# Kernel optimization log

Measured on AMD Instinct MI355X. Metric: run time of the kernel, lower is better.

## Reference

```python
import jax, jax.numpy as jnp
import numpy as np

B, N, D, H = 4, 2048, 1024, 16
HD = D // H  # head_dim = 64


def setup_inputs() -> dict:
    key = jax.random.key(0)
    ks = jax.random.split(key, 7)
    q = jax.random.normal(ks[0], (B, N, D), dtype=jnp.float32)
    k = jax.random.normal(ks[1], (B, N, D), dtype=jnp.float32)
    v = jax.random.normal(ks[2], (B, N, D), dtype=jnp.float32)
    scale = 0.02
    Wq = jax.random.normal(ks[3], (D, D), dtype=jnp.float32) * scale
    Wk = jax.random.normal(ks[4], (D, D), dtype=jnp.float32) * scale
    Wv = jax.random.normal(ks[5], (D, D), dtype=jnp.float32) * scale
    Wo = jax.random.normal(ks[6], (D, D), dtype=jnp.float32) * scale
    return {"q": q, "k": k, "v": v, "Wq": Wq, "Wk": Wk, "Wv": Wv, "Wo": Wo}


def _split_heads(x):
    # b n (h d) -> b h n d
    b, n, d = x.shape
    return x.reshape(b, n, H, HD).transpose(0, 2, 1, 3)


def reference(q, k, v, Wq, Wk, Wv, Wo):
    # nn.Linear(bias=False): y = x @ W.T
    qh = _split_heads(q @ Wq.T)
    kh = _split_heads(k @ Wk.T)
    vh = _split_heads(v @ Wv.T)
    scale = jnp.sqrt(jnp.asarray(HD, dtype=jnp.float32))
    scores = jnp.einsum('bhqd,bhkd->bhqk', qh, kh) / scale  # [B,H,N,N]
    # future (causal) mask: triu(ones, diagonal=1) -> masked_fill(-inf)
    future_mask = jnp.triu(jnp.ones((N, N), dtype=bool), k=1)
    scores = jnp.where(future_mask[None, None, :, :], -jnp.inf, scores)
    attn = jax.nn.softmax(scores, axis=-1)
    out = jnp.einsum('bhqk,bhkd->bhqd', attn, vh)
    # b h n d -> b n (h d)
    out = out.transpose(0, 2, 1, 3).reshape(B, N, D)
    return out @ Wo.T
```

## Files before the change

kernel.cpp:

```cpp
#include <hip/hip_runtime.h>
#include <hip/hip_bf16.h>

#define BATCH 4
#define NSEQ 2048
#define DMODEL 1024
#define NHEAD 16
#define HDIM 64

typedef __attribute__((ext_vector_type(8))) short short8;
typedef __attribute__((ext_vector_type(4))) float f32x4;
typedef __attribute__((ext_vector_type(16))) float f32x16;
typedef __attribute__((ext_vector_type(2))) int int2v;
typedef unsigned short ushort_t;

__device__ __forceinline__ ushort_t f2bf(float f) {
    union { float f; unsigned u; } x; x.f = f;
    unsigned r = x.u + 0x7fffu + ((x.u >> 16) & 1u);
    return (ushort_t)(r >> 16);
}

__device__ __forceinline__ unsigned cvt_pk_bf16(float lo, float hi) {
    unsigned r;
    asm("v_cvt_pk_bf16_f32 %0, %1, %2" : "=v"(r) : "v"(lo), "v"(hi));
    return r;
}

#define GLOAD16(gp, lp) __builtin_amdgcn_global_load_lds(                       \
    (const __attribute__((address_space(1))) unsigned*)(const void*)(gp),       \
    (__attribute__((address_space(3))) unsigned*)(void*)(lp), 16, 0, 0)

__global__ __launch_bounds__(256) void cvt_qkv(const float* __restrict__ q,
                                               const float* __restrict__ k,
                                               const float* __restrict__ v,
                                               ushort_t* __restrict__ out) {
    int bid = blockIdx.x;
    int which = bid >> 12;
    int lb = bid & 4095;
    const float* in = (which == 0) ? q : ((which == 1) ? k : v);
    size_t i = ((size_t)lb * 256 + threadIdx.x) * 8;
    float4 f0 = *(const float4*)(in + i);
    float4 f1 = *(const float4*)(in + i + 4);
    short8 o;
    o[0] = f2bf(f0.x); o[1] = f2bf(f0.y); o[2] = f2bf(f0.z); o[3] = f2bf(f0.w);
    o[4] = f2bf(f1.x); o[5] = f2bf(f1.y); o[6] = f2bf(f1.z); o[7] = f2bf(f1.w);
    *(short8*)(out + (size_t)which * 8388608 + i) = o;
}

__global__ __launch_bounds__(256) void cvt_w4(const float* __restrict__ w0,
                                              const float* __restrict__ w1,
                                              const float* __restrict__ w2,
                                              const float* __restrict__ w3,
                                              ushort_t* __restrict__ out) {
    int bid = blockIdx.x;
    int which = bid >> 9;
    int lb = bid & 511;
    const float* in = (which == 0) ? w0 : ((which == 1) ? w1 : ((which == 2) ? w2 : w3));
    size_t i = ((size_t)lb * 256 + threadIdx.x) * 8;
    float4 f0 = *(const float4*)(in + i);
    float4 f1 = *(const float4*)(in + i + 4);
    short8 o;
    o[0] = f2bf(f0.x); o[1] = f2bf(f0.y); o[2] = f2bf(f0.z); o[3] = f2bf(f0.w);
    o[4] = f2bf(f1.x); o[5] = f2bf(f1.y); o[6] = f2bf(f1.z); o[7] = f2bf(f1.w);
    *(short8*)(out + (size_t)which * 1048576 + i) = o;
}

__device__ __forceinline__ void storeC(float* C, size_t idx, float v) { C[idx] = v; }
__device__ __forceinline__ void storeC(ushort_t* C, size_t idx, float v) { C[idx] = f2bf(v); }

template <typename OutT, int LAYOUT>
__global__ __launch_bounds__(512) void gemm_bt8(const ushort_t* __restrict__ A,
                                                const ushort_t* __restrict__ Bt,
                                                OutT* __restrict__ C,
                                                int M, int N, int K, float alpha) {
    __shared__ ushort_t As[3][256 * 64];
    __shared__ ushort_t Bs[3][128 * 64];

    int tid = threadIdx.x;
    int l = tid & 63, w = tid >> 6;
    int wm = w >> 1, wn = w & 1;
    int lr = l & 15, lk = l >> 4;

    int bid = blockIdx.x;
    int wg = (bid & 7) * 32 + (bid >> 3);
    int nbc = N >> 7;
    int brow = (wg / nbc) << 8;
    int bcol = (wg % nbc) << 7;

    int srow8 = l >> 3;
    int sx = ((l & 7) ^ srow8) * 8;
    const ushort_t* pAsrc = A + (size_t)(brow + w * 32 + srow8) * K + sx;
    const ushort_t* pBsrc = Bt + (size_t)(bcol + w * 16 + srow8) * K + sx;
    const size_t rowK8 = (size_t)8 * K;

    int colx = (lk << 4) ^ ((lr & 7) << 4);
    int abyte = (wm * 64 + lr) * 128 + colx;
    int bbyte = (wn * 64 + lr) * 128 + colx;

    f32x4 acc[4][4] = {};

    const int NT = K >> 6;

#pragma unroll
    for (int c = 0; c < 4; c++) GLOAD16(pAsrc + c * rowK8,      &As[0][(w * 32 + 8 * c) * 64]);
#pragma unroll
    for (int c = 0; c < 2; c++) GLOAD16(pBsrc + c * rowK8,      &Bs[0][(w * 16 + 8 * c) * 64]);
#pragma unroll
    for (int c = 0; c < 4; c++) GLOAD16(pAsrc + c * rowK8 + 64, &As[1][(w * 32 + 8 * c) * 64]);
#pragma unroll
    for (int c = 0; c < 2; c++) GLOAD16(pBsrc + c * rowK8 + 64, &Bs[1][(w * 16 + 8 * c) * 64]);

    int slot = 0, stslot = 2;
    for (int T = 0; T < NT; ++T) {
        if (T < NT - 1) { asm volatile("s_waitcnt vmcnt(6)" ::: "memory"); }
        else            { asm volatile("s_waitcnt vmcnt(0)" ::: "memory"); }
        __builtin_amdgcn_sched_barrier(0);
        __builtin_amdgcn_s_barrier();
        asm volatile("" ::: "memory");

        const char* ab = (const char*)&As[slot][0];
        const char* bb = (const char*)&Bs[slot][0];
        bool stage = (T + 2 < NT);
        int k2 = (T + 2) << 6;

        short8 af[4], bf_[4];
#pragma unroll
        for (int m = 0; m < 4; m++) af[m]  = *(const short8*)(ab + abyte + m * 2048);
#pragma unroll
        for (int n = 0; n < 4; n++) bf_[n] = *(const short8*)(bb + bbyte + n * 2048);
        if (stage) {
            GLOAD16(pAsrc + 0 * rowK8 + k2, &As[stslot][(w * 32 + 0) * 64]);
            GLOAD16(pAsrc + 1 * rowK8 + k2, &As[stslot][(w * 32 + 8) * 64]);
            GLOAD16(pAsrc + 2 * rowK8 + k2, &As[stslot][(w * 32 + 16) * 64]);
        }
        __builtin_amdgcn_s_setprio(1);
#pragma unroll
        for (int m = 0; m < 4; m++)
#pragma unroll
            for (int n = 0; n < 4; n++)
                acc[m][n] = __builtin_amdgcn_mfma_f32_16x16x32_bf16(af[m], bf_[n], acc[m][n], 0, 0, 0);
        __builtin_amdgcn_s_setprio(0);

#pragma unroll
        for (int m = 0; m < 4; m++) af[m]  = *(const short8*)(ab + (abyte ^ 64) + m * 2048);
#pragma unroll
        for (int n = 0; n < 4; n++) bf_[n] = *(const short8*)(bb + (bbyte ^ 64) + n * 2048);
        if (stage) {
            GLOAD16(pAsrc + 3 * rowK8 + k2, &As[stslot][(w * 32 + 24) * 64]);
            GLOAD16(pBsrc + 0 * rowK8 + k2, &Bs[stslot][(w * 16 + 0) * 64]);
            GLOAD16(pBsrc + 1 * rowK8 + k2, &Bs[stslot][(w * 16 + 8) * 64]);
        }
        __builtin_amdgcn_s_setprio(1);
#pragma unroll
        for (int m = 0; m < 4; m++)
#pragma unroll
            for (int n = 0; n < 4; n++)
                acc[m][n] = __builtin_amdgcn_mfma_f32_16x16x32_bf16(af[m], bf_[n], acc[m][n], 0, 0, 0);
        __builtin_amdgcn_s_setprio(0);

        slot = (slot == 2) ? 0 : slot + 1;
        stslot = (stslot == 2) ? 0 : stslot + 1;
    }

#pragma unroll
    for (int m = 0; m < 4; m++)
#pragma unroll
        for (int n = 0; n < 4; n++)
#pragma unroll
            for (int r = 0; r < 4; r++) {
                int row = brow + wm * 64 + m * 16 + lk * 4 + r;
                int col = bcol + wn * 64 + n * 16 + lr;
                float v = acc[m][n][r] * alpha;
                if (LAYOUT == 0) {
                    storeC(C, (size_t)row * N + col, v);
                } else if (LAYOUT == 1) {
                    int b = row >> 11, nn = row & 2047, h = col >> 6, d = col & 63;
                    size_t idx = ((size_t)(b * NHEAD + h) << 17) + ((size_t)(nn >> 5) << 11) +
                                 ((d >> 4) << 9) + ((nn & 31) << 4) + (d & 15);
                    storeC(C, idx, v);
                } else {
                    int b = row >> 11, kk = row & 2047, h = col >> 6, d = col & 63;
                    size_t idx = ((size_t)(b * NHEAD + h) << 17) + ((size_t)(kk >> 6) << 12) +
                                 ((d >> 5) << 11) + (((kk >> 4) & 3) << 9) + ((d & 31) << 4) + (kk & 15);
                    storeC(C, idx, v);
                }
            }
}

__global__ __launch_bounds__(256) void attn_kernel(const ushort_t* __restrict__ Qp,
                                                   const ushort_t* __restrict__ Kp,
                                                   const ushort_t* __restrict__ VT,
                                                   ushort_t* __restrict__ AO) {
    __shared__ float Om[4][64][33];
    __shared__ float Ll[4][32];

    int tid = threadIdx.x;
    int l = tid & 63, w = tid >> 6;
    int lq = l & 31;
    int hi = l >> 5;
    int bid = blockIdx.x;
    int bh = bid & 63;
    int qi = 63 - (bid >> 6);
    int b = bh >> 4, h = bh & 15;

    const size_t hb = (size_t)bh << 17;
    const size_t base = ((size_t)b * NSEQ) * DMODEL + (size_t)h * HDIM;

    int qrow0 = qi * 32;
    int qg = qrow0 + lq;
    int loff = lq * 16 + 8 * hi;

    short8 qf[4];
    {
        const ushort_t* qp = Qp + hb + ((size_t)(qrow0 >> 5) << 11) + loff;
#pragma unroll
        for (int c = 0; c < 4; c++) qf[c] = *(const short8*)(qp + (c << 9));
    }

    f32x16 O0 = {}, O1 = {};
    float lrun = 0.f;

    int jmax = (qrow0 >> 6) + 1;
    for (int j = w; j < jmax; j += 4) {
        int k0 = j << 6;
        short8 kf0[4], kf1[4];
        {
            const ushort_t* kp = Kp + hb + ((size_t)(2 * j) << 11) + loff;
#pragma unroll
            for (int c = 0; c < 4; c++) { kf0[c] = *(const short8*)(kp + (c << 9));
                                          kf1[c] = *(const short8*)(kp + 2048 + (c << 9)); }
        }
        short8 vf0[4], vf1[4];
        {
            const ushort_t* vp = VT + hb + ((size_t)j << 12) + loff;
#pragma unroll
            for (int c = 0; c < 4; c++) { vf0[c] = *(const short8*)(vp + (c << 9));
                                          vf1[c] = *(const short8*)(vp + 2048 + (c << 9)); }
        }
        f32x16 S0 = {}, S1 = {};
#pragma unroll
        for (int c = 0; c < 4; c++) S0 = __builtin_amdgcn_mfma_f32_32x32x16_bf16(kf0[c], qf[c], S0, 0, 0, 0);
#pragma unroll
        for (int c = 0; c < 4; c++) S1 = __builtin_amdgcn_mfma_f32_32x32x16_bf16(kf1[c], qf[c], S1, 0, 0, 0);

        if (j == jmax - 1) {
#pragma unroll
            for (int r = 0; r < 16; r++) {
                int kk = k0 + (r & 3) + 8 * (r >> 2) + 4 * hi;
                if (kk > qg)      S0[r] = -1e30f;
                if (kk + 32 > qg) S1[r] = -1e30f;
            }
        }
        float rs0 = 0.f, rs1 = 0.f;
#pragma unroll
        for (int r = 0; r < 16; r++) {
            S0[r] = __builtin_amdgcn_exp2f(S0[r] - 32.f);
            S1[r] = __builtin_amdgcn_exp2f(S1[r] - 32.f);
            rs0 += S0[r]; rs1 += S1[r];
        }
        float rs = rs0 + rs1;
        rs += __shfl_xor(rs, 32);
        lrun += rs;
        unsigned pw0[8], pw1[8];
#pragma unroll
        for (int jj = 0; jj < 8; jj++) {
            pw0[jj] = cvt_pk_bf16(S0[2 * jj], S0[2 * jj + 1]);
            pw1[jj] = cvt_pk_bf16(S1[2 * jj], S1[2 * jj + 1]);
        }
        short8 pfr[4];
        {
            union U { unsigned u[4]; short8 s; };
            int2v a, bb;
            a  = __builtin_amdgcn_permlane32_swap((int)pw0[0], (int)pw0[2], false, false);
            bb = __builtin_amdgcn_permlane32_swap((int)pw0[1], (int)pw0[3], false, false);
            U u0; u0.u[0] = (unsigned)a[0]; u0.u[1] = (unsigned)bb[0];
                  u0.u[2] = (unsigned)a[1]; u0.u[3] = (unsigned)bb[1];
            pfr[0] = u0.s;
            a  = __builtin_amdgcn_permlane32_swap((int)pw0[4], (int)pw0[6], false, false);
            bb = __builtin_amdgcn_permlane32_swap((int)pw0[5], (int)pw0[7], false, false);
            U u1; u1.u[0] = (unsigned)a[0]; u1.u[1] = (unsigned)bb[0];
                  u1.u[2] = (unsigned)a[1]; u1.u[3] = (unsigned)bb[1];
            pfr[1] = u1.s;
            a  = __builtin_amdgcn_permlane32_swap((int)pw1[0], (int)pw1[2], false, false);
            bb = __builtin_amdgcn_permlane32_swap((int)pw1[1], (int)pw1[3], false, false);
            U u2; u2.u[0] = (unsigned)a[0]; u2.u[1] = (unsigned)bb[0];
                  u2.u[2] = (unsigned)a[1]; u2.u[3] = (unsigned)bb[1];
            pfr[2] = u2.s;
            a  = __builtin_amdgcn_permlane32_swap((int)pw1[4], (int)pw1[6], false, false);
            bb = __builtin_amdgcn_permlane32_swap((int)pw1[5], (int)pw1[7], false, false);
            U u3; u3.u[0] = (unsigned)a[0]; u3.u[1] = (unsigned)bb[0];
                  u3.u[2] = (unsigned)a[1]; u3.u[3] = (unsigned)bb[1];
            pfr[3] = u3.s;
        }
#pragma unroll
        for (int c = 0; c < 4; c++) O0 = __builtin_amdgcn_mfma_f32_32x32x16_bf16(vf0[c], pfr[c], O0, 0, 0, 0);
#pragma unroll
        for (int c = 0; c < 4; c++) O1 = __builtin_amdgcn_mfma_f32_32x32x16_bf16(vf1[c], pfr[c], O1, 0, 0, 0);
    }
    if (hi == 0) Ll[w][lq] = lrun;
#pragma unroll
    for (int r = 0; r < 16; r++) {
        int d0r = (r & 3) + 8 * (r >> 2) + 4 * hi;
        Om[w][d0r][lq]      = O0[r];
        Om[w][d0r + 32][lq] = O1[r];
    }
    __syncthreads();
    int tq = tid >> 3, td = (tid & 7) * 8;
    float lt = Ll[0][tq] + Ll[1][tq] + Ll[2][tq] + Ll[3][tq];
    float inv = 1.f / lt;
    unsigned ow[4];
#pragma unroll
    for (int i = 0; i < 4; i++) {
        float oa = (Om[0][td + 2 * i][tq] + Om[1][td + 2 * i][tq] +
                    Om[2][td + 2 * i][tq] + Om[3][td + 2 * i][tq]) * inv;
        float ob = (Om[0][td + 2 * i + 1][tq] + Om[1][td + 2 * i + 1][tq] +
                    Om[2][td + 2 * i + 1][tq] + Om[3][td + 2 * i + 1][tq]) * inv;
        ow[i] = cvt_pk_bf16(oa, ob);
    }
    uint4 uv = {ow[0], ow[1], ow[2], ow[3]};
    *(uint4*)(AO + base + (size_t)(qrow0 + tq) * DMODEL + td) = uv;
}

extern "C" void kernel_launch(void* const* d_in, const int* in_sizes, int n_in,
                              void* d_out, int out_size, void* d_ws, size_t ws_size,
                              hipStream_t stream) {
    const float* q  = (const float*)d_in[0];
    const float* k  = (const float*)d_in[1];
    const float* v  = (const float*)d_in[2];
    const float* Wq = (const float*)d_in[3];
    const float* Wk = (const float*)d_in[4];
    const float* Wv = (const float*)d_in[5];
    const float* Wo = (const float*)d_in[6];
    float* out = (float*)d_out;

    const size_t BND = (size_t)BATCH * NSEQ * DMODEL;
    const size_t WSZ = (size_t)DMODEL * DMODEL;
    const size_t need = (7 * BND + 4 * WSZ) * sizeof(ushort_t);
    if (ws_size < need) return;

    ushort_t* ws  = (ushort_t*)d_ws;
    ushort_t* qb  = ws;
    ushort_t* kb  = qb + BND;
    ushort_t* vb  = kb + BND;
    ushort_t* Qp  = vb + BND;
    ushort_t* Kp  = Qp + BND;
    ushort_t* VT  = Kp + BND;
    ushort_t* AO  = VT + BND;
    ushort_t* Wqb = AO + BND;

    const int M = BATCH * NSEQ;

    cvt_qkv<<<3 * 4096, 256, 0, stream>>>(q, k, v, qb);
    cvt_w4<<<4 * 512, 256, 0, stream>>>(Wq, Wk, Wv, Wo, Wqb);

    int gblocks = (M / 256) * (DMODEL / 128);
    gemm_bt8<ushort_t, 1><<<gblocks, 512, 0, stream>>>(qb, Wqb, Qp, M, DMODEL, DMODEL, 0.18033688011112043f);
    gemm_bt8<ushort_t, 1><<<gblocks, 512, 0, stream>>>(kb, Wqb + WSZ, Kp, M, DMODEL, DMODEL, 1.0f);
    gemm_bt8<ushort_t, 2><<<gblocks, 512, 0, stream>>>(vb, Wqb + 2 * WSZ, VT, M, DMODEL, DMODEL, 1.0f);

    attn_kernel<<<64 * 64, 256, 0, stream>>>(Qp, Kp, VT, AO);

    gemm_bt8<float, 0><<<gblocks, 512, 0, stream>>>(AO, Wqb + 3 * WSZ, out, M, DMODEL, DMODEL, 1.0f);
}
```

Measured before the change: 181.9 us.

## Fuse conversion and QKV projection launches; give each attention wave its own query tile

```diff
diff --git a/kernel.cpp b/kernel.cpp
--- a/kernel.cpp
+++ b/kernel.cpp
@@ -29,43 +29,42 @@
     (const __attribute__((address_space(1))) unsigned*)(const void*)(gp),       \
     (__attribute__((address_space(3))) unsigned*)(void*)(lp), 16, 0, 0)
 
-__global__ __launch_bounds__(256) void cvt_qkv(const float* __restrict__ q,
+__global__ __launch_bounds__(256) void cvt_all(const float* __restrict__ q,
                                                const float* __restrict__ k,
                                                const float* __restrict__ v,
-                                               ushort_t* __restrict__ out) {
+                                               const float* __restrict__ w0,
+                                               const float* __restrict__ w1,
+                                               const float* __restrict__ w2,
+                                               const float* __restrict__ w3,
+                                               ushort_t* __restrict__ oqkv,
+                                               ushort_t* __restrict__ ow) {
     int bid = blockIdx.x;
-    int which = bid >> 12;
-    int lb = bid & 4095;
-    const float* in = (which == 0) ? q : ((which == 1) ? k : v);
-    size_t i = ((size_t)lb * 256 + threadIdx.x) * 8;
+    const float* in;
+    ushort_t* out;
+    size_t i;
+    if (bid < 12288) {
+        int which = bid >> 12, lb = bid & 4095;
+        in = (which == 0) ? q : ((which == 1) ? k : v);
+        i = ((size_t)lb * 256 + threadIdx.x) * 8;
+        out = oqkv + (size_t)which * 8388608;
+    } else {
+        int wb = bid - 12288;
+        int which = wb >> 9, lb = wb & 511;
+        in = (which == 0) ? w0 : ((which == 1) ? w1 : ((which == 2) ? w2 : w3));
+        i = ((size_t)lb * 256 + threadIdx.x) * 8;
+        out = ow + (size_t)which * 1048576;
+    }
     float4 f0 = *(const float4*)(in + i);
     float4 f1 = *(const float4*)(in + i + 4);
     short8 o;
     o[0] = f2bf(f0.x); o[1] = f2bf(f0.y); o[2] = f2bf(f0.z); o[3] = f2bf(f0.w);
     o[4] = f2bf(f1.x); o[5] = f2bf(f1.y); o[6] = f2bf(f1.z); o[7] = f2bf(f1.w);
-    *(short8*)(out + (size_t)which * 8388608 + i) = o;
-}
-
-__global__ __launch_bounds__(256) void cvt_w4(const float* __restrict__ w0,
-                                              const float* __restrict__ w1,
-                                              const float* __restrict__ w2,
-                                              const float* __restrict__ w3,
-                                              ushort_t* __restrict__ out) {
-    int bid = blockIdx.x;
-    int which = bid >> 9;
-    int lb = bid & 511;
-    const float* in = (which == 0) ? w0 : ((which == 1) ? w1 : ((which == 2) ? w2 : w3));
-    size_t i = ((size_t)lb * 256 + threadIdx.x) * 8;
-    float4 f0 = *(const float4*)(in + i);
-    float4 f1 = *(const float4*)(in + i + 4);
-    short8 o;
-    o[0] = f2bf(f0.x); o[1] = f2bf(f0.y); o[2] = f2bf(f0.z); o[3] = f2bf(f0.w);
-    o[4] = f2bf(f1.x); o[5] = f2bf(f1.y); o[6] = f2bf(f1.z); o[7] = f2bf(f1.w);
-    *(short8*)(out + (size_t)which * 1048576 + i) = o;
+    *(short8*)(out + i) = o;
 }
 
 __device__ __forceinline__ void storeC(float* C, size_t idx, float v) { C[idx] = v; }
 __device__ __forceinline__ void storeC(ushort_t* C, size_t idx, float v) { C[idx] = f2bf(v); }
+
 
 template <typename OutT, int LAYOUT>
 __global__ __launch_bounds__(512) void gemm_bt8(const ushort_t* __restrict__ A,
@@ -97,7 +96,6 @@
     int bbyte = (wn * 64 + lr) * 128 + colx;
 
     f32x4 acc[4][4] = {};
-
     const int NT = K >> 6;
 
 #pragma unroll
@@ -186,20 +184,141 @@
             }
 }
 
-__global__ __launch_bounds__(256) void attn_kernel(const ushort_t* __restrict__ Qp,
-                                                   const ushort_t* __restrict__ Kp,
-                                                   const ushort_t* __restrict__ VT,
-                                                   ushort_t* __restrict__ AO) {
-    __shared__ float Om[4][64][33];
-    __shared__ float Ll[4][32];
-
+__global__ __launch_bounds__(512) void proj_gemm(const ushort_t* __restrict__ qb,
+                                                 const ushort_t* __restrict__ kb,
+                                                 const ushort_t* __restrict__ vb,
+                                                 const ushort_t* __restrict__ W4,
+                                                 ushort_t* __restrict__ Qp,
+                                                 ushort_t* __restrict__ Kp,
+                                                 ushort_t* __restrict__ VTp) {
+    __shared__ ushort_t As[3][256 * 64];
+    __shared__ ushort_t Bs[3][128 * 64];
+
+    const int K = DMODEL, N = DMODEL;
+    int sel = blockIdx.x >> 8;
+    const ushort_t* A  = (sel == 0) ? qb : ((sel == 1) ? kb : vb);
+    const ushort_t* Bt = W4 + (size_t)sel * (DMODEL * DMODEL);
+    ushort_t* C = (sel == 0) ? Qp : ((sel == 1) ? Kp : VTp);
+    float alpha = (sel == 0) ? 0.18033688011112043f : 1.0f;
+
+    int tid = threadIdx.x;
+    int l = tid & 63, w = tid >> 6;
+    int wm = w >> 1, wn = w & 1;
+    int lr = l & 15, lk = l >> 4;
+
+    int bid = blockIdx.x & 255;
+    int wg = (bid & 7) * 32 + (bid >> 3);
+    int brow = (wg >> 3) << 8;
+    int bcol = (wg & 7) << 7;
+
+    int srow8 = l >> 3;
+    int sx = ((l & 7) ^ srow8) * 8;
+    const ushort_t* pAsrc = A + (size_t)(brow + w * 32 + srow8) * K + sx;
+    const ushort_t* pBsrc = Bt + (size_t)(bcol + w * 16 + srow8) * K + sx;
+    const size_t rowK8 = (size_t)8 * K;
+
+    int colx = (lk << 4) ^ ((lr & 7) << 4);
+    int abyte = (wm * 64 + lr) * 128 + colx;
+    int bbyte = (wn * 64 + lr) * 128 + colx;
+
+    f32x4 acc[4][4] = {};
+    const int NT = K >> 6;
+
+#pragma unroll
+    for (int c = 0; c < 4; c++) GLOAD16(pAsrc + c * rowK8,      &As[0][(w * 32 + 8 * c) * 64]);
+#pragma unroll
+    for (int c = 0; c < 2; c++) GLOAD16(pBsrc + c * rowK8,      &Bs[0][(w * 16 + 8 * c) * 64]);
+#pragma unroll
+    for (int c = 0; c < 4; c++) GLOAD16(pAsrc + c * rowK8 + 64, &As[1][(w * 32 + 8 * c) * 64]);
+#pragma unroll
+    for (int c = 0; c < 2; c++) GLOAD16(pBsrc + c * rowK8 + 64, &Bs[1][(w * 16 + 8 * c) * 64]);
+
+    int slot = 0, stslot = 2;
+    for (int T = 0; T < NT; ++T) {
+        if (T < NT - 1) { asm volatile("s_waitcnt vmcnt(6)" ::: "memory"); }
+        else            { asm volatile("s_waitcnt vmcnt(0)" ::: "memory"); }
+        __builtin_amdgcn_sched_barrier(0);
+        __builtin_amdgcn_s_barrier();
+        asm volatile("" ::: "memory");
+
+        const char* ab = (const char*)&As[slot][0];
+        const char* bb = (const char*)&Bs[slot][0];
+        bool stage = (T + 2 < NT);
+        int k2 = (T + 2) << 6;
+
+        short8 af[4], bf_[4];
+#pragma unroll
+        for (int m = 0; m < 4; m++) af[m]  = *(const short8*)(ab + abyte + m * 2048);
+#pragma unroll
+        for (int n = 0; n < 4; n++) bf_[n] = *(const short8*)(bb + bbyte + n * 2048);
+        if (stage) {
+            GLOAD16(pAsrc + 0 * rowK8 + k2, &As[stslot][(w * 32 + 0) * 64]);
+            GLOAD16(pAsrc + 1 * rowK8 + k2, &As[stslot][(w * 32 + 8) * 64]);
+            GLOAD16(pAsrc + 2 * rowK8 + k2, &As[stslot][(w * 32 + 16) * 64]);
+        }
+        __builtin_amdgcn_s_setprio(1);
+#pragma unroll
+        for (int m = 0; m < 4; m++)
+#pragma unroll
+            for (int n = 0; n < 4; n++)
+                acc[m][n] = __builtin_amdgcn_mfma_f32_16x16x32_bf16(af[m], bf_[n], acc[m][n], 0, 0, 0);
+        __builtin_amdgcn_s_setprio(0);
+
+#pragma unroll
+        for (int m = 0; m < 4; m++) af[m]  = *(const short8*)(ab + (abyte ^ 64) + m * 2048);
+#pragma unroll
+        for (int n = 0; n < 4; n++) bf_[n] = *(const short8*)(bb + (bbyte ^ 64) + n * 2048);
+        if (stage) {
+            GLOAD16(pAsrc + 3 * rowK8 + k2, &As[stslot][(w * 32 + 24) * 64]);
+            GLOAD16(pBsrc + 0 * rowK8 + k2, &Bs[stslot][(w * 16 + 0) * 64]);
+            GLOAD16(pBsrc + 1 * rowK8 + k2, &Bs[stslot][(w * 16 + 8) * 64]);
+        }
+        __builtin_amdgcn_s_setprio(1);
+#pragma unroll
+        for (int m = 0; m < 4; m++)
+#pragma unroll
+            for (int n = 0; n < 4; n++)
+                acc[m][n] = __builtin_amdgcn_mfma_f32_16x16x32_bf16(af[m], bf_[n], acc[m][n], 0, 0, 0);
+        __builtin_amdgcn_s_setprio(0);
+
+        slot = (slot == 2) ? 0 : slot + 1;
+        stslot = (stslot == 2) ? 0 : stslot + 1;
+    }
+
+#pragma unroll
+    for (int m = 0; m < 4; m++)
+#pragma unroll
+        for (int n = 0; n < 4; n++)
+#pragma unroll
+            for (int r = 0; r < 4; r++) {
+                int row = brow + wm * 64 + m * 16 + lk * 4 + r;
+                int col = bcol + wn * 64 + n * 16 + lr;
+                float v = acc[m][n][r] * alpha;
+                int b = row >> 11, nn = row & 2047, h = col >> 6, d = col & 63;
+                size_t idx;
+                if (sel != 2) {
+                    idx = ((size_t)(b * NHEAD + h) << 17) + ((size_t)(nn >> 5) << 11) +
+                          ((d >> 4) << 9) + ((nn & 31) << 4) + (d & 15);
+                } else {
+                    idx = ((size_t)(b * NHEAD + h) << 17) + ((size_t)(nn >> 6) << 12) +
+                          ((d >> 5) << 11) + (((nn >> 4) & 3) << 9) + ((d & 31) << 4) + (nn & 15);
+                }
+                C[idx] = f2bf(v);
+            }
+}
+
+__global__ __launch_bounds__(256, 4) void attn_kernel(const ushort_t* __restrict__ Qp,
+                                                      const ushort_t* __restrict__ Kp,
+                                                      const ushort_t* __restrict__ VT,
+                                                      ushort_t* __restrict__ AO) {
     int tid = threadIdx.x;
     int l = tid & 63, w = tid >> 6;
     int lq = l & 31;
     int hi = l >> 5;
     int bid = blockIdx.x;
     int bh = bid & 63;
-    int qi = 63 - (bid >> 6);
+    int o = ((bid >> 6) << 2) + w;
+    int qi = 63 - o;
     int b = bh >> 4, h = bh & 15;
 
     const size_t hb = (size_t)bh << 17;
@@ -211,7 +330,7 @@
 
     short8 qf[4];
     {
-        const ushort_t* qp = Qp + hb + ((size_t)(qrow0 >> 5) << 11) + loff;
+        const ushort_t* qp = Qp + hb + ((size_t)qi << 11) + loff;
 #pragma unroll
         for (int c = 0; c < 4; c++) qf[c] = *(const short8*)(qp + (c << 9));
     }
@@ -219,8 +338,8 @@
     f32x16 O0 = {}, O1 = {};
     float lrun = 0.f;
 
-    int jmax = (qrow0 >> 6) + 1;
-    for (int j = w; j < jmax; j += 4) {
+    int jmax = (qi >> 1) + 1;
+    for (int j = 0; j < jmax; ++j) {
         int k0 = j << 6;
         short8 kf0[4], kf1[4];
         {
@@ -296,28 +415,19 @@
 #pragma unroll
         for (int c = 0; c < 4; c++) O1 = __builtin_amdgcn_mfma_f32_32x32x16_bf16(vf1[c], pfr[c], O1, 0, 0, 0);
     }
-    if (hi == 0) Ll[w][lq] = lrun;
-#pragma unroll
-    for (int r = 0; r < 16; r++) {
-        int d0r = (r & 3) + 8 * (r >> 2) + 4 * hi;
-        Om[w][d0r][lq]      = O0[r];
-        Om[w][d0r + 32][lq] = O1[r];
-    }
-    __syncthreads();
-    int tq = tid >> 3, td = (tid & 7) * 8;
-    float lt = Ll[0][tq] + Ll[1][tq] + Ll[2][tq] + Ll[3][tq];
-    float inv = 1.f / lt;
-    unsigned ow[4];
-#pragma unroll
-    for (int i = 0; i < 4; i++) {
-        float oa = (Om[0][td + 2 * i][tq] + Om[1][td + 2 * i][tq] +
-                    Om[2][td + 2 * i][tq] + Om[3][td + 2 * i][tq]) * inv;
-        float ob = (Om[0][td + 2 * i + 1][tq] + Om[1][td + 2 * i + 1][tq] +
-                    Om[2][td + 2 * i + 1][tq] + Om[3][td + 2 * i + 1][tq]) * inv;
-        ow[i] = cvt_pk_bf16(oa, ob);
-    }
-    uint4 uv = {ow[0], ow[1], ow[2], ow[3]};
-    *(uint4*)(AO + base + (size_t)(qrow0 + tq) * DMODEL + td) = uv;
+    float inv = 1.f / lrun;
+    size_t rowoff = base + (size_t)qg * DMODEL;
+#pragma unroll
+    for (int q4 = 0; q4 < 4; q4++) {
+        unsigned a0 = cvt_pk_bf16(O0[4 * q4] * inv,     O0[4 * q4 + 1] * inv);
+        unsigned a1 = cvt_pk_bf16(O0[4 * q4 + 2] * inv, O0[4 * q4 + 3] * inv);
+        uint2 ua = {a0, a1};
+        *(uint2*)(AO + rowoff + 8 * q4 + 4 * hi) = ua;
+        unsigned b0 = cvt_pk_bf16(O1[4 * q4] * inv,     O1[4 * q4 + 1] * inv);
+        unsigned b1 = cvt_pk_bf16(O1[4 * q4 + 2] * inv, O1[4 * q4 + 3] * inv);
+        uint2 ub = {b0, b1};
+        *(uint2*)(AO + rowoff + 32 + 8 * q4 + 4 * hi) = ub;
+    }
 }
 
 extern "C" void kernel_launch(void* const* d_in, const int* in_sizes, int n_in,
@@ -349,15 +459,11 @@
 
     const int M = BATCH * NSEQ;
 
-    cvt_qkv<<<3 * 4096, 256, 0, stream>>>(q, k, v, qb);
-    cvt_w4<<<4 * 512, 256, 0, stream>>>(Wq, Wk, Wv, Wo, Wqb);
-
-    int gblocks = (M / 256) * (DMODEL / 128);
-    gemm_bt8<ushort_t, 1><<<gblocks, 512, 0, stream>>>(qb, Wqb, Qp, M, DMODEL, DMODEL, 0.18033688011112043f);
-    gemm_bt8<ushort_t, 1><<<gblocks, 512, 0, stream>>>(kb, Wqb + WSZ, Kp, M, DMODEL, DMODEL, 1.0f);
-    gemm_bt8<ushort_t, 2><<<gblocks, 512, 0, stream>>>(vb, Wqb + 2 * WSZ, VT, M, DMODEL, DMODEL, 1.0f);
-
-    attn_kernel<<<64 * 64, 256, 0, stream>>>(Qp, Kp, VT, AO);
-
-    gemm_bt8<float, 0><<<gblocks, 512, 0, stream>>>(AO, Wqb + 3 * WSZ, out, M, DMODEL, DMODEL, 1.0f);
-}
+    cvt_all<<<14336, 256, 0, stream>>>(q, k, v, Wq, Wk, Wv, Wo, qb, Wqb);
+
+    proj_gemm<<<768, 512, 0, stream>>>(qb, kb, vb, Wqb, Qp, Kp, VT);
+
+    attn_kernel<<<1024, 256, 0, stream>>>(Qp, Kp, VT, AO);
+
+    gemm_bt8<float, 0><<<256, 512, 0, stream>>>(AO, Wqb + 3 * WSZ, out, M, DMODEL, DMODEL, 1.0f);
+}
```

Result: slower. 190.3 us (+4.6%).

## Pair causal query tiles per wave and share K/V loads, dropping cross-wave reduction

Applied to the files above, without the earlier changes.

```diff
diff --git a/kernel.cpp b/kernel.cpp
--- a/kernel.cpp
+++ b/kernel.cpp
@@ -97,7 +97,6 @@
     int bbyte = (wn * 64 + lr) * 128 + colx;
 
     f32x4 acc[4][4] = {};
-
     const int NT = K >> 6;
 
 #pragma unroll
@@ -186,138 +185,202 @@
             }
 }
 
-__global__ __launch_bounds__(256) void attn_kernel(const ushort_t* __restrict__ Qp,
-                                                   const ushort_t* __restrict__ Kp,
-                                                   const ushort_t* __restrict__ VT,
-                                                   ushort_t* __restrict__ AO) {
-    __shared__ float Om[4][64][33];
-    __shared__ float Ll[4][32];
-
+__global__ __launch_bounds__(256, 2) void attn_kernel(const ushort_t* __restrict__ Qp,
+                                                      const ushort_t* __restrict__ Kp,
+                                                      const ushort_t* __restrict__ VT,
+                                                      ushort_t* __restrict__ AO) {
     int tid = threadIdx.x;
     int l = tid & 63, w = tid >> 6;
     int lq = l & 31;
     int hi = l >> 5;
-    int bid = blockIdx.x;
-    int bh = bid & 63;
-    int qi = 63 - (bid >> 6);
-    int b = bh >> 4, h = bh & 15;
+    int p = blockIdx.x * 4 + w;
+    int bh = p >> 5;
+    int pi = p & 31;
+    int qiL = pi, qiH = 63 - pi;
+    int jlo = (qiL >> 1) + 1;
+    int jhi = (qiH >> 1) + 1;
+    int b = bh >> 4;
 
     const size_t hb = (size_t)bh << 17;
-    const size_t base = ((size_t)b * NSEQ) * DMODEL + (size_t)h * HDIM;
-
-    int qrow0 = qi * 32;
-    int qg = qrow0 + lq;
+    const size_t base = ((size_t)b * NSEQ) * DMODEL + (size_t)(bh & 15) * HDIM;
+
+    int qgL = qiL * 32 + lq;
+    int qgH = qiH * 32 + lq;
     int loff = lq * 16 + 8 * hi;
 
-    short8 qf[4];
+    short8 qfL[4], qfH[4];
     {
-        const ushort_t* qp = Qp + hb + ((size_t)(qrow0 >> 5) << 11) + loff;
-#pragma unroll
-        for (int c = 0; c < 4; c++) qf[c] = *(const short8*)(qp + (c << 9));
+        const ushort_t* qpL = Qp + hb + ((size_t)qiL << 11) + loff;
+        const ushort_t* qpH = Qp + hb + ((size_t)qiH << 11) + loff;
+#pragma unroll
+        for (int c = 0; c < 4; c++) { qfL[c] = *(const short8*)(qpL + (c << 9));
+                                      qfH[c] = *(const short8*)(qpH + (c << 9)); }
     }
 
-    f32x16 O0 = {}, O1 = {};
-    float lrun = 0.f;
-
-    int jmax = (qrow0 >> 6) + 1;
-    for (int j = w; j < jmax; j += 4) {
+    f32x16 OL0 = {}, OL1 = {}, OH0 = {}, OH1 = {};
+    float lrunL = 0.f, lrunH = 0.f;
+
+    for (int j = 0; j < jhi; ++j) {
         int k0 = j << 6;
-        short8 kf0[4], kf1[4];
+        short8 kf0[4], kf1[4], vf0[4], vf1[4];
         {
             const ushort_t* kp = Kp + hb + ((size_t)(2 * j) << 11) + loff;
-#pragma unroll
-            for (int c = 0; c < 4; c++) { kf0[c] = *(const short8*)(kp + (c << 9));
-                                          kf1[c] = *(const short8*)(kp + 2048 + (c << 9)); }
-        }
-        short8 vf0[4], vf1[4];
+            const ushort_t* vp = VT + hb + ((size_t)j << 12) + loff;
+#pragma unroll
+            for (int c = 0; c < 4; c++) {
+                kf0[c] = *(const short8*)(kp + (c << 9));
+                kf1[c] = *(const short8*)(kp + 2048 + (c << 9));
+                vf0[c] = *(const short8*)(vp + (c << 9));
+                vf1[c] = *(const short8*)(vp + 2048 + (c << 9));
+            }
+        }
         {
-            const ushort_t* vp = VT + hb + ((size_t)j << 12) + loff;
-#pragma unroll
-            for (int c = 0; c < 4; c++) { vf0[c] = *(const short8*)(vp + (c << 9));
-                                          vf1[c] = *(const short8*)(vp + 2048 + (c << 9)); }
-        }
-        f32x16 S0 = {}, S1 = {};
-#pragma unroll
-        for (int c = 0; c < 4; c++) S0 = __builtin_amdgcn_mfma_f32_32x32x16_bf16(kf0[c], qf[c], S0, 0, 0, 0);
-#pragma unroll
-        for (int c = 0; c < 4; c++) S1 = __builtin_amdgcn_mfma_f32_32x32x16_bf16(kf1[c], qf[c], S1, 0, 0, 0);
-
-        if (j == jmax - 1) {
+            f32x16 S0 = {}, S1 = {};
+#pragma unroll
+            for (int c = 0; c < 4; c++) S0 = __builtin_amdgcn_mfma_f32_32x32x16_bf16(kf0[c], qfH[c], S0, 0, 0, 0);
+#pragma unroll
+            for (int c = 0; c < 4; c++) S1 = __builtin_amdgcn_mfma_f32_32x32x16_bf16(kf1[c], qfH[c], S1, 0, 0, 0);
+            if (j == jhi - 1) {
+#pragma unroll
+                for (int r = 0; r < 16; r++) {
+                    int kk = k0 + (r & 3) + 8 * (r >> 2) + 4 * hi;
+                    if (kk > qgH)      S0[r] = -1e30f;
+                    if (kk + 32 > qgH) S1[r] = -1e30f;
+                }
+            }
+            float rs0 = 0.f, rs1 = 0.f;
 #pragma unroll
             for (int r = 0; r < 16; r++) {
-                int kk = k0 + (r & 3) + 8 * (r >> 2) + 4 * hi;
-                if (kk > qg)      S0[r] = -1e30f;
-                if (kk + 32 > qg) S1[r] = -1e30f;
-            }
-        }
-        float rs0 = 0.f, rs1 = 0.f;
-#pragma unroll
-        for (int r = 0; r < 16; r++) {
-            S0[r] = __builtin_amdgcn_exp2f(S0[r] - 32.f);
-            S1[r] = __builtin_amdgcn_exp2f(S1[r] - 32.f);
-            rs0 += S0[r]; rs1 += S1[r];
-        }
-        float rs = rs0 + rs1;
-        rs += __shfl_xor(rs, 32);
-        lrun += rs;
-        unsigned pw0[8], pw1[8];
-#pragma unroll
-        for (int jj = 0; jj < 8; jj++) {
-            pw0[jj] = cvt_pk_bf16(S0[2 * jj], S0[2 * jj + 1]);
-            pw1[jj] = cvt_pk_bf16(S1[2 * jj], S1[2 * jj + 1]);
-        }
-        short8 pfr[4];
-        {
-            union U { unsigned u[4]; short8 s; };
-            int2v a, bb;
-            a  = __builtin_amdgcn_permlane32_swap((int)pw0[0], (int)pw0[2], false, false);
-            bb = __builtin_amdgcn_permlane32_swap((int)pw0[1], (int)pw0[3], false, false);
-            U u0; u0.u[0] = (unsigned)a[0]; u0.u[1] = (unsigned)bb[0];
-                  u0.u[2] = (unsigned)a[1]; u0.u[3] = (unsigned)bb[1];
-            pfr[0] = u0.s;
-            a  = __builtin_amdgcn_permlane32_swap((int)pw0[4], (int)pw0[6], false, false);
-            bb = __builtin_amdgcn_permlane32_swap((int)pw0[5], (int)pw0[7], false, false);
-            U u1; u1.u[0] = (unsigned)a[0]; u1.u[1] = (unsigned)bb[0];
-                  u1.u[2] = (unsigned)a[1]; u1.u[3] = (unsigned)bb[1];
-            pfr[1] = u1.s;
-            a  = __builtin_amdgcn_permlane32_swap((int)pw1[0], (int)pw1[2], false, false);
-            bb = __builtin_amdgcn_permlane32_swap((int)pw1[1], (int)pw1[3], false, false);
-            U u2; u2.u[0] = (unsigned)a[0]; u2.u[1] = (unsigned)bb[0];
-                  u2.u[2] = (unsigned)a[1]; u2.u[3] = (unsigned)bb[1];
-            pfr[2] = u2.s;
-            a  = __builtin_amdgcn_permlane32_swap((int)pw1[4], (int)pw1[6], false, false);
-            bb = __builtin_amdgcn_permlane32_swap((int)pw1[5], (int)pw1[7], false, false);
-            U u3; u3.u[0] = (unsigned)a[0]; u3.u[1] = (unsigned)bb[0];
-                  u3.u[2] = (unsigned)a[1]; u3.u[3] = (unsigned)bb[1];
-            pfr[3] = u3.s;
-        }
-#pragma unroll
-        for (int c = 0; c < 4; c++) O0 = __builtin_amdgcn_mfma_f32_32x32x16_bf16(vf0[c], pfr[c], O0, 0, 0, 0);
-#pragma unroll
-        for (int c = 0; c < 4; c++) O1 = __builtin_amdgcn_mfma_f32_32x32x16_bf16(vf1[c], pfr[c], O1, 0, 0, 0);
+                S0[r] = __builtin_amdgcn_exp2f(S0[r] - 32.f);
+                S1[r] = __builtin_amdgcn_exp2f(S1[r] - 32.f);
+                rs0 += S0[r]; rs1 += S1[r];
+            }
+            float rs = rs0 + rs1;
+            rs += __shfl_xor(rs, 32);
+            lrunH += rs;
+            unsigned pw0[8], pw1[8];
+#pragma unroll
+            for (int jj = 0; jj < 8; jj++) {
+                pw0[jj] = cvt_pk_bf16(S0[2 * jj], S0[2 * jj + 1]);
+                pw1[jj] = cvt_pk_bf16(S1[2 * jj], S1[2 * jj + 1]);
+            }
+            short8 pfr[4];
+            {
+                union U { unsigned u[4]; short8 s; };
+                int2v a, bb;
+                a  = __builtin_amdgcn_permlane32_swap((int)pw0[0], (int)pw0[2], false, false);
+                bb = __builtin_amdgcn_permlane32_swap((int)pw0[1], (int)pw0[3], false, false);
+                U u0; u0.u[0] = (unsigned)a[0]; u0.u[1] = (unsigned)bb[0];
+                      u0.u[2] = (unsigned)a[1]; u0.u[3] = (unsigned)bb[1];
+                pfr[0] = u0.s;
+                a  = __builtin_amdgcn_permlane32_swap((int)pw0[4], (int)pw0[6], false, false);
+                bb = __builtin_amdgcn_permlane32_swap((int)pw0[5], (int)pw0[7], false, false);
+                U u1; u1.u[0] = (unsigned)a[0]; u1.u[1] = (unsigned)bb[0];
+                      u1.u[2] = (unsigned)a[1]; u1.u[3] = (unsigned)bb[1];
+                pfr[1] = u1.s;
+                a  = __builtin_amdgcn_permlane32_swap((int)pw1[0], (int)pw1[2], false, false);
+                bb = __builtin_amdgcn_permlane32_swap((int)pw1[1], (int)pw1[3], false, false);
+                U u2; u2.u[0] = (unsigned)a[0]; u2.u[1] = (unsigned)bb[0];
+                      u2.u[2] = (unsigned)a[1]; u2.u[3] = (unsigned)bb[1];
+                pfr[2] = u2.s;
+                a  = __builtin_amdgcn_permlane32_swap((int)pw1[4], (int)pw1[6], false, false);
+                bb = __builtin_amdgcn_permlane32_swap((int)pw1[5], (int)pw1[7], false, false);
+                U u3; u3.u[0] = (unsigned)a[0]; u3.u[1] = (unsigned)bb[0];
+                      u3.u[2] = (unsigned)a[1]; u3.u[3] = (unsigned)bb[1];
+                pfr[3] = u3.s;
+            }
+#pragma unroll
+            for (int c = 0; c < 4; c++) OH0 = __builtin_amdgcn_mfma_f32_32x32x16_bf16(vf0[c], pfr[c], OH0, 0, 0, 0);
+#pragma unroll
+            for (int c = 0; c < 4; c++) OH1 = __builtin_amdgcn_mfma_f32_32x32x16_bf16(vf1[c], pfr[c], OH1, 0, 0, 0);
+        }
+        if (j < jlo) {
+            f32x16 S0 = {}, S1 = {};
+#pragma unroll
+            for (int c = 0; c < 4; c++) S0 = __builtin_amdgcn_mfma_f32_32x32x16_bf16(kf0[c], qfL[c], S0, 0, 0, 0);
+#pragma unroll
+            for (int c = 0; c < 4; c++) S1 = __builtin_amdgcn_mfma_f32_32x32x16_bf16(kf1[c], qfL[c], S1, 0, 0, 0);
+            if (j == jlo - 1) {
+#pragma unroll
+                for (int r = 0; r < 16; r++) {
+                    int kk = k0 + (r & 3) + 8 * (r >> 2) + 4 * hi;
+                    if (kk > qgL)      S0[r] = -1e30f;
+                    if (kk + 32 > qgL) S1[r] = -1e30f;
+                }
+            }
+            float rs0 = 0.f, rs1 = 0.f;
+#pragma unroll
+            for (int r = 0; r < 16; r++) {
+                S0[r] = __builtin_amdgcn_exp2f(S0[r] - 32.f);
+                S1[r] = __builtin_amdgcn_exp2f(S1[r] - 32.f);
+                rs0 += S0[r]; rs1 += S1[r];
+            }
+            float rs = rs0 + rs1;
+            rs += __shfl_xor(rs, 32);
+            lrunL += rs;
+            unsigned pw0[8], pw1[8];
+#pragma unroll
+            for (int jj = 0; jj < 8; jj++) {
+                pw0[jj] = cvt_pk_bf16(S0[2 * jj], S0[2 * jj + 1]);
+                pw1[jj] = cvt_pk_bf16(S1[2 * jj], S1[2 * jj + 1]);
+            }
+            short8 pfr[4];
+            {
+                union U { unsigned u[4]; short8 s; };
+                int2v a, bb;
+                a  = __builtin_amdgcn_permlane32_swap((int)pw0[0], (int)pw0[2], false, false);
+                bb = __builtin_amdgcn_permlane32_swap((int)pw0[1], (int)pw0[3], false, false);
+                U u0; u0.u[0] = (unsigned)a[0]; u0.u[1] = (unsigned)bb[0];
+                      u0.u[2] = (unsigned)a[1]; u0.u[3] = (unsigned)bb[1];
+                pfr[0] = u0.s;
+                a  = __builtin_amdgcn_permlane32_swap((int)pw0[4], (int)pw0[6], false, false);
+                bb = __builtin_amdgcn_permlane32_swap((int)pw0[5], (int)pw0[7], false, false);
+                U u1; u1.u[0] = (unsigned)a[0]; u1.u[1] = (unsigned)bb[0];
+                      u1.u[2] = (unsigned)a[1]; u1.u[3] = (unsigned)bb[1];
+                pfr[1] = u1.s;
+                a  = __builtin_amdgcn_permlane32_swap((int)pw1[0], (int)pw1[2], false, false);
+                bb = __builtin_amdgcn_permlane32_swap((int)pw1[1], (int)pw1[3], false, false);
+                U u2; u2.u[0] = (unsigned)a[0]; u2.u[1] = (unsigned)bb[0];
+                      u2.u[2] = (unsigned)a[1]; u2.u[3] = (unsigned)bb[1];
+                pfr[2] = u2.s;
+                a  = __builtin_amdgcn_permlane32_swap((int)pw1[4], (int)pw1[6], false, false);
+                bb = __builtin_amdgcn_permlane32_swap((int)pw1[5], (int)pw1[7], false, false);
+                U u3; u3.u[0] = (unsigned)a[0]; u3.u[1] = (unsigned)bb[0];
+                      u3.u[2] = (unsigned)a[1]; u3.u[3] = (unsigned)bb[1];
+                pfr[3] = u3.s;
+            }
+#pragma unroll
+            for (int c = 0; c < 4; c++) OL0 = __builtin_amdgcn_mfma_f32_32x32x16_bf16(vf0[c], pfr[c], OL0, 0, 0, 0);
+#pragma unroll
+            for (int c = 0; c < 4; c++) OL1 = __builtin_amdgcn_mfma_f32_32x32x16_bf16(vf1[c], pfr[c], OL1, 0, 0, 0);
+        }
     }
-    if (hi == 0) Ll[w][lq] = lrun;
-#pragma unroll
-    for (int r = 0; r < 16; r++) {
-        int d0r = (r & 3) + 8 * (r >> 2) + 4 * hi;
-        Om[w][d0r][lq]      = O0[r];
-        Om[w][d0r + 32][lq] = O1[r];
+    {
+        float inv = 1.f / lrunL;
+        size_t rowoff = base + (size_t)qgL * DMODEL;
+#pragma unroll
+        for (int q4 = 0; q4 < 4; q4++) {
+            uint2 ua = {cvt_pk_bf16(OL0[4 * q4] * inv,     OL0[4 * q4 + 1] * inv),
+                        cvt_pk_bf16(OL0[4 * q4 + 2] * inv, OL0[4 * q4 + 3] * inv)};
+            *(uint2*)(AO + rowoff + 8 * q4 + 4 * hi) = ua;
+            uint2 ub = {cvt_pk_bf16(OL1[4 * q4] * inv,     OL1[4 * q4 + 1] * inv),
+                        cvt_pk_bf16(OL1[4 * q4 + 2] * inv, OL1[4 * q4 + 3] * inv)};
+            *(uint2*)(AO + rowoff + 32 + 8 * q4 + 4 * hi) = ub;
+        }
     }
-    __syncthreads();
-    int tq = tid >> 3, td = (tid & 7) * 8;
-    float lt = Ll[0][tq] + Ll[1][tq] + Ll[2][tq] + Ll[3][tq];
-    float inv = 1.f / lt;
-    unsigned ow[4];
-#pragma unroll
-    for (int i = 0; i < 4; i++) {
-        float oa = (Om[0][td + 2 * i][tq] + Om[1][td + 2 * i][tq] +
-                    Om[2][td + 2 * i][tq] + Om[3][td + 2 * i][tq]) * inv;
-        float ob = (Om[0][td + 2 * i + 1][tq] + Om[1][td + 2 * i + 1][tq] +
-                    Om[2][td + 2 * i + 1][tq] + Om[3][td + 2 * i + 1][tq]) * inv;
-        ow[i] = cvt_pk_bf16(oa, ob);
+    {
+        float inv = 1.f / lrunH;
+        size_t rowoff = base + (size_t)qgH * DMODEL;
+#pragma unroll
+        for (int q4 = 0; q4 < 4; q4++) {
+            uint2 ua = {cvt_pk_bf16(OH0[4 * q4] * inv,     OH0[4 * q4 + 1] * inv),
+                        cvt_pk_bf16(OH0[4 * q4 + 2] * inv, OH0[4 * q4 + 3] * inv)};
+            *(uint2*)(AO + rowoff + 8 * q4 + 4 * hi) = ua;
+            uint2 ub = {cvt_pk_bf16(OH1[4 * q4] * inv,     OH1[4 * q4 + 1] * inv),
+                        cvt_pk_bf16(OH1[4 * q4 + 2] * inv, OH1[4 * q4 + 3] * inv)};
+            *(uint2*)(AO + rowoff + 32 + 8 * q4 + 4 * hi) = ub;
+        }
     }
-    uint4 uv = {ow[0], ow[1], ow[2], ow[3]};
-    *(uint4*)(AO + base + (size_t)(qrow0 + tq) * DMODEL + td) = uv;
 }
 
 extern "C" void kernel_launch(void* const* d_in, const int* in_sizes, int n_in,
@@ -357,7 +420,7 @@
     gemm_bt8<ushort_t, 1><<<gblocks, 512, 0, stream>>>(kb, Wqb + WSZ, Kp, M, DMODEL, DMODEL, 1.0f);
     gemm_bt8<ushort_t, 2><<<gblocks, 512, 0, stream>>>(vb, Wqb + 2 * WSZ, VT, M, DMODEL, DMODEL, 1.0f);
 
-    attn_kernel<<<64 * 64, 256, 0, stream>>>(Qp, Kp, VT, AO);
-
-    gemm_bt8<float, 0><<<gblocks, 512, 0, stream>>>(AO, Wqb + 3 * WSZ, out, M, DMODEL, DMODEL, 1.0f);
-}
+    attn_kernel<<<512, 256, 0, stream>>>(Qp, Kp, VT, AO);
+
+    gemm_bt8<float, 0><<<256, 512, 0, stream>>>(AO, Wqb + 3 * WSZ, out, M, DMODEL, DMODEL, 1.0f);
+}
```

Result: faster. 171.2 us (-5.9%).

## Give each attention wave its own query tile with causal load balancing

Applied to the files above, without the earlier changes.

```diff
diff --git a/kernel.cpp b/kernel.cpp
--- a/kernel.cpp
+++ b/kernel.cpp
@@ -97,7 +97,6 @@
     int bbyte = (wn * 64 + lr) * 128 + colx;
 
     f32x4 acc[4][4] = {};
-
     const int NT = K >> 6;
 
 #pragma unroll
@@ -186,32 +185,66 @@
             }
 }
 
-__global__ __launch_bounds__(256) void attn_kernel(const ushort_t* __restrict__ Qp,
-                                                   const ushort_t* __restrict__ Kp,
-                                                   const ushort_t* __restrict__ VT,
-                                                   ushort_t* __restrict__ AO) {
-    __shared__ float Om[4][64][33];
-    __shared__ float Ll[4][32];
-
+__device__ __forceinline__ void pack_pfr(const f32x16& S0, const f32x16& S1, short8 (&pfr)[4]) {
+    unsigned pw0[8], pw1[8];
+#pragma unroll
+    for (int jj = 0; jj < 8; jj++) {
+        pw0[jj] = cvt_pk_bf16(S0[2 * jj], S0[2 * jj + 1]);
+        pw1[jj] = cvt_pk_bf16(S1[2 * jj], S1[2 * jj + 1]);
+    }
+    union U { unsigned u[4]; short8 s; };
+    int2v a, bb;
+    a  = __builtin_amdgcn_permlane32_swap((int)pw0[0], (int)pw0[2], false, false);
+    bb = __builtin_amdgcn_permlane32_swap((int)pw0[1], (int)pw0[3], false, false);
+    U u0; u0.u[0] = (unsigned)a[0]; u0.u[1] = (unsigned)bb[0];
+          u0.u[2] = (unsigned)a[1]; u0.u[3] = (unsigned)bb[1];
+    pfr[0] = u0.s;
+    a  = __builtin_amdgcn_permlane32_swap((int)pw0[4], (int)pw0[6], false, false);
+    bb = __builtin_amdgcn_permlane32_swap((int)pw0[5], (int)pw0[7], false, false);
+    U u1; u1.u[0] = (unsigned)a[0]; u1.u[1] = (unsigned)bb[0];
+          u1.u[2] = (unsigned)a[1]; u1.u[3] = (unsigned)bb[1];
+    pfr[1] = u1.s;
+    a  = __builtin_amdgcn_permlane32_swap((int)pw1[0], (int)pw1[2], false, false);
+    bb = __builtin_amdgcn_permlane32_swap((int)pw1[1], (int)pw1[3], false, false);
+    U u2; u2.u[0] = (unsigned)a[0]; u2.u[1] = (unsigned)bb[0];
+          u2.u[2] = (unsigned)a[1]; u2.u[3] = (unsigned)bb[1];
+    pfr[2] = u2.s;
+    a  = __builtin_amdgcn_permlane32_swap((int)pw1[4], (int)pw1[6], false, false);
+    bb = __builtin_amdgcn_permlane32_swap((int)pw1[5], (int)pw1[7], false, false);
+    U u3; u3.u[0] = (unsigned)a[0]; u3.u[1] = (unsigned)bb[0];
+          u3.u[2] = (unsigned)a[1]; u3.u[3] = (unsigned)bb[1];
+    pfr[3] = u3.s;
+}
+
+__global__ __launch_bounds__(256, 4) void attn_kernel(const ushort_t* __restrict__ Qp,
+                                                      const ushort_t* __restrict__ Kp,
+                                                      const ushort_t* __restrict__ VT,
+                                                      ushort_t* __restrict__ AO) {
     int tid = threadIdx.x;
     int l = tid & 63, w = tid >> 6;
     int lq = l & 31;
     int hi = l >> 5;
     int bid = blockIdx.x;
-    int bh = bid & 63;
-    int qi = 63 - (bid >> 6);
-    int b = bh >> 4, h = bh & 15;
+    int x = bid & 7;
+    int g = bid >> 3;
+    int bh = x + 8 * (g & 7);
+    int pp = g >> 3;
+    int pi = 2 * pp + (w >> 1);
+    int qi = (w & 1) ? (63 - pi) : pi;
+    int b = bh >> 4;
 
     const size_t hb = (size_t)bh << 17;
-    const size_t base = ((size_t)b * NSEQ) * DMODEL + (size_t)h * HDIM;
-
-    int qrow0 = qi * 32;
-    int qg = qrow0 + lq;
+    const size_t base = ((size_t)b * NSEQ) * DMODEL + (size_t)(bh & 15) * HDIM;
+
+    int qg = qi * 32 + lq;
     int loff = lq * 16 + 8 * hi;
+
+    const ushort_t* kpbase = Kp + hb + loff;
+    const ushort_t* vpbase = VT + hb + loff;
 
     short8 qf[4];
     {
-        const ushort_t* qp = Qp + hb + ((size_t)(qrow0 >> 5) << 11) + loff;
+        const ushort_t* qp = Qp + hb + ((size_t)qi << 11) + loff;
 #pragma unroll
         for (int c = 0; c < 4; c++) qf[c] = *(const short8*)(qp + (c << 9));
     }
@@ -219,22 +252,20 @@
     f32x16 O0 = {}, O1 = {};
     float lrun = 0.f;
 
-    int jmax = (qrow0 >> 6) + 1;
-    for (int j = w; j < jmax; j += 4) {
+    int jmax = (qi >> 1) + 1;
+    for (int j = 0; j < jmax; ++j) {
         int k0 = j << 6;
-        short8 kf0[4], kf1[4];
+        short8 kf0[4], kf1[4], vf0[4], vf1[4];
         {
-            const ushort_t* kp = Kp + hb + ((size_t)(2 * j) << 11) + loff;
-#pragma unroll
-            for (int c = 0; c < 4; c++) { kf0[c] = *(const short8*)(kp + (c << 9));
-                                          kf1[c] = *(const short8*)(kp + 2048 + (c << 9)); }
-        }
-        short8 vf0[4], vf1[4];
-        {
-            const ushort_t* vp = VT + hb + ((size_t)j << 12) + loff;
-#pragma unroll
-            for (int c = 0; c < 4; c++) { vf0[c] = *(const short8*)(vp + (c << 9));
-                                          vf1[c] = *(const short8*)(vp + 2048 + (c << 9)); }
+            const ushort_t* kp = kpbase + ((size_t)(2 * j) << 11);
+            const ushort_t* vp = vpbase + ((size_t)j << 12);
+#pragma unroll
+            for (int c = 0; c < 4; c++) {
+                kf0[c] = *(const short8*)(kp + (c << 9));
+                kf1[c] = *(const short8*)(kp + 2048 + (c << 9));
+                vf0[c] = *(const short8*)(vp + (c << 9));
+                vf1[c] = *(const short8*)(vp + 2048 + (c << 9));
+            }
         }
         f32x16 S0 = {}, S1 = {};
 #pragma unroll
@@ -250,74 +281,33 @@
                 if (kk + 32 > qg) S1[r] = -1e30f;
             }
         }
-        float rs0 = 0.f, rs1 = 0.f;
+        float rs = 0.f;
 #pragma unroll
         for (int r = 0; r < 16; r++) {
             S0[r] = __builtin_amdgcn_exp2f(S0[r] - 32.f);
             S1[r] = __builtin_amdgcn_exp2f(S1[r] - 32.f);
-            rs0 += S0[r]; rs1 += S1[r];
-        }
-        float rs = rs0 + rs1;
+            rs += S0[r] + S1[r];
+        }
         rs += __shfl_xor(rs, 32);
         lrun += rs;
-        unsigned pw0[8], pw1[8];
-#pragma unroll
-        for (int jj = 0; jj < 8; jj++) {
-            pw0[jj] = cvt_pk_bf16(S0[2 * jj], S0[2 * jj + 1]);
-            pw1[jj] = cvt_pk_bf16(S1[2 * jj], S1[2 * jj + 1]);
-        }
         short8 pfr[4];
-        {
-            union U { unsigned u[4]; short8 s; };
-            int2v a, bb;
-            a  = __builtin_amdgcn_permlane32_swap((int)pw0[0], (int)pw0[2], false, false);
-            bb = __builtin_amdgcn_permlane32_swap((int)pw0[1], (int)pw0[3], false, false);
-            U u0; u0.u[0] = (unsigned)a[0]; u0.u[1] = (unsigned)bb[0];
-                  u0.u[2] = (unsigned)a[1]; u0.u[3] = (unsigned)bb[1];
-            pfr[0] = u0.s;
-            a  = __builtin_amdgcn_permlane32_swap((int)pw0[4], (int)pw0[6], false, false);
-            bb = __builtin_amdgcn_permlane32_swap((int)pw0[5], (int)pw0[7], false, false);
-            U u1; u1.u[0] = (unsigned)a[0]; u1.u[1] = (unsigned)bb[0];
-                  u1.u[2] = (unsigned)a[1]; u1.u[3] = (unsigned)bb[1];
-            pfr[1] = u1.s;
-            a  = __builtin_amdgcn_permlane32_swap((int)pw1[0], (int)pw1[2], false, false);
-            bb = __builtin_amdgcn_permlane32_swap((int)pw1[1], (int)pw1[3], false, false);
-            U u2; u2.u[0] = (unsigned)a[0]; u2.u[1] = (unsigned)bb[0];
-                  u2.u[2] = (unsigned)a[1]; u2.u[3] = (unsigned)bb[1];
-            pfr[2] = u2.s;
-            a  = __builtin_amdgcn_permlane32_swap((int)pw1[4], (int)pw1[6], false, false);
-            bb = __builtin_amdgcn_permlane32_swap((int)pw1[5], (int)pw1[7], false, false);
-            U u3; u3.u[0] = (unsigned)a[0]; u3.u[1] = (unsigned)bb[0];
-                  u3.u[2] = (unsigned)a[1]; u3.u[3] = (unsigned)bb[1];
-            pfr[3] = u3.s;
-        }
+        pack_pfr(S0, S1, pfr);
 #pragma unroll
         for (int c = 0; c < 4; c++) O0 = __builtin_amdgcn_mfma_f32_32x32x16_bf16(vf0[c], pfr[c], O0, 0, 0, 0);
 #pragma unroll
         for (int c = 0; c < 4; c++) O1 = __builtin_amdgcn_mfma_f32_32x32x16_bf16(vf1[c], pfr[c], O1, 0, 0, 0);
     }
-    if (hi == 0) Ll[w][lq] = lrun;
-#pragma unroll
-    for (int r = 0; r < 16; r++) {
-        int d0r = (r & 3) + 8 * (r >> 2) + 4 * hi;
-        Om[w][d0r][lq]      = O0[r];
-        Om[w][d0r + 32][lq] = O1[r];
-    }
-    __syncthreads();
-    int tq = tid >> 3, td = (tid & 7) * 8;
-    float lt = Ll[0][tq] + Ll[1][tq] + Ll[2][tq] + Ll[3][tq];
-    float inv = 1.f / lt;
-    unsigned ow[4];
-#pragma unroll
-    for (int i = 0; i < 4; i++) {
-        float oa = (Om[0][td + 2 * i][tq] + Om[1][td + 2 * i][tq] +
-                    Om[2][td + 2 * i][tq] + Om[3][td + 2 * i][tq]) * inv;
-        float ob = (Om[0][td + 2 * i + 1][tq] + Om[1][td + 2 * i + 1][tq] +
-                    Om[2][td + 2 * i + 1][tq] + Om[3][td + 2 * i + 1][tq]) * inv;
-        ow[i] = cvt_pk_bf16(oa, ob);
-    }
-    uint4 uv = {ow[0], ow[1], ow[2], ow[3]};
-    *(uint4*)(AO + base + (size_t)(qrow0 + tq) * DMODEL + td) = uv;
+    float inv = 1.f / lrun;
+    size_t rowoff = base + (size_t)qg * DMODEL;
+#pragma unroll
+    for (int q4 = 0; q4 < 4; q4++) {
+        uint2 ua = {cvt_pk_bf16(O0[4 * q4] * inv,     O0[4 * q4 + 1] * inv),
+                    cvt_pk_bf16(O0[4 * q4 + 2] * inv, O0[4 * q4 + 3] * inv)};
+        *(uint2*)(AO + rowoff + 8 * q4 + 4 * hi) = ua;
+        uint2 ub = {cvt_pk_bf16(O1[4 * q4] * inv,     O1[4 * q4 + 1] * inv),
+                    cvt_pk_bf16(O1[4 * q4 + 2] * inv, O1[4 * q4 + 3] * inv)};
+        *(uint2*)(AO + rowoff + 32 + 8 * q4 + 4 * hi) = ub;
+    }
 }
 
 extern "C" void kernel_launch(void* const* d_in, const int* in_sizes, int n_in,
@@ -357,7 +347,7 @@
     gemm_bt8<ushort_t, 1><<<gblocks, 512, 0, stream>>>(kb, Wqb + WSZ, Kp, M, DMODEL, DMODEL, 1.0f);
     gemm_bt8<ushort_t, 2><<<gblocks, 512, 0, stream>>>(vb, Wqb + 2 * WSZ, VT, M, DMODEL, DMODEL, 1.0f);
 
-    attn_kernel<<<64 * 64, 256, 0, stream>>>(Qp, Kp, VT, AO);
+    attn_kernel<<<1024, 256, 0, stream>>>(Qp, Kp, VT, AO);
 
     gemm_bt8<float, 0><<<gblocks, 512, 0, stream>>>(AO, Wqb + 3 * WSZ, out, M, DMODEL, DMODEL, 1.0f);
 }
```

New measurement: 183.4 us. About the same (+0.8%).
